# Optimization experiments

Hardware: AMD Instinct MI355X
Metric: run time of the kernel (lower is better)

The kernel has to match this reference:

```python
import jax, jax.numpy as jnp
import numpy as np

B, F, T, D = 65536, 1024, 64, 6


def setup_inputs() -> dict:
    key = jax.random.key(0)
    k0, k1, k2, k3 = jax.random.split(key, 4)
    x = jax.random.normal(k0, (B, F), dtype=jnp.float32)
    splits = jax.random.normal(k1, (T, D, F), dtype=jnp.float32)
    thresholds = jax.random.normal(k2, (T, D), dtype=jnp.float32)
    values = jax.random.normal(k3, (T, 2 ** D), dtype=jnp.float32)
    return {"x": x, "splits": splits, "thresholds": thresholds, "values": values}


def reference(x, splits, thresholds, values):
    # Since split_idx = depth % max_depth = depth, each level's split is path-independent.
    # bit_d = 1 means 'right' (score > threshold); node after D steps = 2^D - 1 + code,
    # leaf_idx = node - 2^D = code - 1 (torch negative indexing => mod 2^D).
    T_, D_, _ = splits.shape
    scores = jnp.einsum('bf,tdf->tbd', x, splits)          # (T, B, D)
    bits = (scores > thresholds[:, None, :]).astype(jnp.int32)
    pow2 = (2 ** jnp.arange(D_ - 1, -1, -1)).astype(jnp.int32)  # weight 2^(D-1-d)
    code = jnp.sum(bits * pow2, axis=-1)                   # (T, B)
    leaf = jnp.mod(code - 1, 2 ** D_)                      # (T, B)
    out_t = jnp.take_along_axis(values, leaf, axis=1)      # (T, B)
    return jnp.mean(out_t, axis=0)[:, None]                # (B, 1)
```

## Files before the change

kernel.cpp:

```cpp
#include <hip/hip_runtime.h>

#define BTOT 65536
#define FDIM 1024
#define TNUM 64
#define DNUM 6

#define BAND      1.5e-3f
#define GCUT      1.5e-4f
#define HEDGE_MAX 1.35f
#define CAP       8192

typedef unsigned int u32;
typedef unsigned long long u64;
using f32x4  = __attribute__((ext_vector_type(4))) float;
using bf16x8 = __attribute__((ext_vector_type(8))) short;

__device__ __forceinline__ short f32_to_bf16(float v) {
    u32 bits = __float_as_uint(v);
    bits += 0x7FFFu + ((bits >> 16) & 1u);
    return (short)(bits >> 16);
}
__device__ __forceinline__ float bf16_to_f32(short h) {
    return __uint_as_float(((u32)(unsigned short)h) << 16);
}

#define RPITCH 40
#define A_HI_S 0
#define A_LO_S (64 * RPITCH)
#define B_HI_S (128 * RPITCH)
#define B_LO_S (128 * RPITCH + 384 * RPITCH)
#define SMEM_SHORTS (128 * RPITCH + 2 * 384 * RPITCH)
#define B_BASE_BYTES (2 * B_HI_S)
#define BTILE_BYTES  61440
#define PRE_OFFSET   65536

__global__ void pre_split(const float* __restrict__ splits,
                          short* __restrict__ pre) {
    const int q  = blockIdx.x * 256 + threadIdx.x;
    const int r  = q >> 8;
    const int c4 = q & 255;
    const float4 v = *(const float4*)(splits + (size_t)r * FDIM + c4 * 4);
    const int ks = c4 >> 3;
    const int c  = (c4 & 7) * 4;
    short* tile = pre + (size_t)ks * (BTILE_BYTES / 2);
    const float vv[4] = {v.x, v.y, v.z, v.w};
    short hh[4], ll[4];
    #pragma unroll
    for (int e = 0; e < 4; ++e) {
        hh[e] = f32_to_bf16(vv[e]);
        ll[e] = f32_to_bf16(vv[e] - bf16_to_f32(hh[e]));
    }
    *(short4*)(tile + r * RPITCH + c)               = make_short4(hh[0], hh[1], hh[2], hh[3]);
    *(short4*)(tile + 384 * RPITCH + r * RPITCH + c) = make_short4(ll[0], ll[1], ll[2], ll[3]);
}

__global__ __launch_bounds__(256, 2)
void forest_mfma(const float* __restrict__ x,
                 const float* __restrict__ splits,
                 const float* __restrict__ thresholds,
                 const float* __restrict__ values,
                 float* __restrict__ out,
                 u32* __restrict__ gcnt,
                 u32* __restrict__ cands,
                 const short* __restrict__ pre,
                 const int use_pre) {
    __shared__ __align__(16) short smem[SMEM_SHORTS];

    const int tid  = threadIdx.x;
    const int lane = tid & 63;
    const int w    = tid >> 6;
    const int fr   = lane & 15;
    const int fq   = lane >> 4;
    const int b0   = blockIdx.x * 64;

    f32x4 acc[6][4];
    #pragma unroll
    for (int tt = 0; tt < 6; ++tt)
        #pragma unroll
        for (int bt = 0; bt < 4; ++bt) acc[tt][bt] = (f32x4)0.0f;

    #pragma unroll
    for (int j = 0; j < 2; ++j) {
        const int q = tid + j * 256, ra = q >> 3, c4 = q & 7;
        const float4 v = *(const float4*)(x + (size_t)(b0 + ra) * FDIM + c4 * 4);
        const float vv[4] = {v.x, v.y, v.z, v.w};
        short hh[4], ll[4];
        #pragma unroll
        for (int e = 0; e < 4; ++e) {
            hh[e] = f32_to_bf16(vv[e]);
            ll[e] = f32_to_bf16(vv[e] - bf16_to_f32(hh[e]));
        }
        *(short4*)(smem + A_HI_S + ra * RPITCH + c4 * 4) = make_short4(hh[0], hh[1], hh[2], hh[3]);
        *(short4*)(smem + A_LO_S + ra * RPITCH + c4 * 4) = make_short4(ll[0], ll[1], ll[2], ll[3]);
    }

    if (use_pre) {
        {
            const char* srcb = (const char*)pre;
            #pragma unroll
            for (int j = 0; j < 15; ++j) {
                const int ub = (j * 256 + w * 64) * 16;
                __builtin_amdgcn_global_load_lds(
                    (const void*)(srcb + ub + (lane << 4)),
                    (void*)((char*)smem + B_BASE_BYTES + ub),
                    16, 0, 0);
            }
        }
        __syncthreads();

        for (int ks = 0; ks < 32; ++ks) {
            bf16x8 sh[6], sl[6], xh[4], xl[4];
            #pragma unroll
            for (int tt = 0; tt < 6; ++tt) {
                const int ro = (w * 96 + tt * 16 + fr) * RPITCH + fq * 8;
                sh[tt] = *(const bf16x8*)(smem + B_HI_S + ro);
                sl[tt] = *(const bf16x8*)(smem + B_LO_S + ro);
            }
            #pragma unroll
            for (int bt = 0; bt < 4; ++bt) {
                const int ro = (bt * 16 + fr) * RPITCH + fq * 8;
                xh[bt] = *(const bf16x8*)(smem + A_HI_S + ro);
                xl[bt] = *(const bf16x8*)(smem + A_LO_S + ro);
            }
            float4 pa[2];
            if (ks < 31) {
                #pragma unroll
                for (int j = 0; j < 2; ++j) {
                    const int q = tid + j * 256, ra = q >> 3, c4 = q & 7;
                    pa[j] = *(const float4*)(x + (size_t)(b0 + ra) * FDIM + (ks + 1) * 32 + c4 * 4);
                }
            }
            __syncthreads();

            if (ks < 31) {
                const char* srcb = (const char*)pre + (size_t)(ks + 1) * BTILE_BYTES;
                #pragma unroll
                for (int j = 0; j < 15; ++j) {
                    const int ub = (j * 256 + w * 64) * 16;
                    __builtin_amdgcn_global_load_lds(
                        (const void*)(srcb + ub + (lane << 4)),
                        (void*)((char*)smem + B_BASE_BYTES + ub),
                        16, 0, 0);
                }
            }
            #pragma unroll
            for (int tt = 0; tt < 6; ++tt)
                #pragma unroll
                for (int bt = 0; bt < 4; ++bt) {
                    acc[tt][bt] = __builtin_amdgcn_mfma_f32_16x16x32_bf16(sh[tt], xh[bt], acc[tt][bt], 0, 0, 0);
                    acc[tt][bt] = __builtin_amdgcn_mfma_f32_16x16x32_bf16(sh[tt], xl[bt], acc[tt][bt], 0, 0, 0);
                    acc[tt][bt] = __builtin_amdgcn_mfma_f32_16x16x32_bf16(sl[tt], xh[bt], acc[tt][bt], 0, 0, 0);
                }
            if (ks < 31) {
                #pragma unroll
                for (int j = 0; j < 2; ++j) {
                    const int q = tid + j * 256, ra = q >> 3, c4 = q & 7;
                    const float vv[4] = {pa[j].x, pa[j].y, pa[j].z, pa[j].w};
                    short hh[4], ll[4];
                    #pragma unroll
                    for (int e = 0; e < 4; ++e) {
                        hh[e] = f32_to_bf16(vv[e]);
                        ll[e] = f32_to_bf16(vv[e] - bf16_to_f32(hh[e]));
                    }
                    *(short4*)(smem + A_HI_S + ra * RPITCH + c4 * 4) = make_short4(hh[0], hh[1], hh[2], hh[3]);
                    *(short4*)(smem + A_LO_S + ra * RPITCH + c4 * 4) = make_short4(ll[0], ll[1], ll[2], ll[3]);
                }
            }
            __syncthreads();
        }
    } else {
        for (int ks = 0; ks < 32; ++ks) {
            const int k0 = ks * 32;
            if (ks) {
                __syncthreads();
                #pragma unroll
                for (int j = 0; j < 2; ++j) {
                    const int q = tid + j * 256, ra = q >> 3, c4 = q & 7;
                    const float4 v = *(const float4*)(x + (size_t)(b0 + ra) * FDIM + k0 + c4 * 4);
                    const float vv[4] = {v.x, v.y, v.z, v.w};
                    short hh[4], ll[4];
                    #pragma unroll
                    for (int e = 0; e < 4; ++e) {
                        hh[e] = f32_to_bf16(vv[e]);
                        ll[e] = f32_to_bf16(vv[e] - bf16_to_f32(hh[e]));
                    }
                    *(short4*)(smem + A_HI_S + ra * RPITCH + c4 * 4) = make_short4(hh[0], hh[1], hh[2], hh[3]);
                    *(short4*)(smem + A_LO_S + ra * RPITCH + c4 * 4) = make_short4(ll[0], ll[1], ll[2], ll[3]);
                }
            }
            #pragma unroll
            for (int j = 0; j < 12; ++j) {
                const int q = tid + j * 256, rb = q >> 3, c4 = q & 7;
                const float4 v = *(const float4*)(splits + (size_t)rb * FDIM + k0 + c4 * 4);
                const float vv[4] = {v.x, v.y, v.z, v.w};
                short hh[4], ll[4];
                #pragma unroll
                for (int e = 0; e < 4; ++e) {
                    hh[e] = f32_to_bf16(vv[e]);
                    ll[e] = f32_to_bf16(vv[e] - bf16_to_f32(hh[e]));
                }
                *(short4*)(smem + B_HI_S + rb * RPITCH + c4 * 4) = make_short4(hh[0], hh[1], hh[2], hh[3]);
                *(short4*)(smem + B_LO_S + rb * RPITCH + c4 * 4) = make_short4(ll[0], ll[1], ll[2], ll[3]);
            }
            __syncthreads();
            bf16x8 sh[6], sl[6], xh[4], xl[4];
            #pragma unroll
            for (int tt = 0; tt < 6; ++tt) {
                const int ro = (w * 96 + tt * 16 + fr) * RPITCH + fq * 8;
                sh[tt] = *(const bf16x8*)(smem + B_HI_S + ro);
                sl[tt] = *(const bf16x8*)(smem + B_LO_S + ro);
            }
            #pragma unroll
            for (int bt = 0; bt < 4; ++bt) {
                const int ro = (bt * 16 + fr) * RPITCH + fq * 8;
                xh[bt] = *(const bf16x8*)(smem + A_HI_S + ro);
                xl[bt] = *(const bf16x8*)(smem + A_LO_S + ro);
            }
            #pragma unroll
            for (int tt = 0; tt < 6; ++tt)
                #pragma unroll
                for (int bt = 0; bt < 4; ++bt) {
                    acc[tt][bt] = __builtin_amdgcn_mfma_f32_16x16x32_bf16(sh[tt], xh[bt], acc[tt][bt], 0, 0, 0);
                    acc[tt][bt] = __builtin_amdgcn_mfma_f32_16x16x32_bf16(sh[tt], xl[bt], acc[tt][bt], 0, 0, 0);
                    acc[tt][bt] = __builtin_amdgcn_mfma_f32_16x16x32_bf16(sl[tt], xh[bt], acc[tt][bt], 0, 0, 0);
                }
        }
        __syncthreads();
    }

    float th[6][4];
    #pragma unroll
    for (int tt = 0; tt < 6; ++tt)
        #pragma unroll
        for (int reg = 0; reg < 4; ++reg)
            th[tt][reg] = thresholds[w * 96 + tt * 16 + fq * 4 + reg];

    float* psum = (float*)smem;

    #pragma unroll
    for (int bt = 0; bt < 4; ++bt) {
        u64 bal[6][4];
        u32 bandmask = 0;
        #pragma unroll
        for (int tt = 0; tt < 6; ++tt)
            #pragma unroll
            for (int reg = 0; reg < 4; ++reg) {
                const float df = acc[tt][bt][reg] - th[tt][reg];
                bal[tt][reg] = __ballot(df > 0.0f);
                if (__builtin_expect(fabsf(df) < BAND, 0))
                    bandmask |= 1u << ((tt * 16 + fq * 4 + reg) / 6);
            }
        bandmask |= __shfl_xor(bandmask, 16);
        bandmask |= __shfl_xor(bandmask, 32);

        float partial = 0.0f;
        #pragma unroll
        for (int jj = 0; jj < 4; ++jj) {
            const int j = fq * 4 + jj;
            int code = 0;
            #pragma unroll
            for (int d = 0; d < DNUM; ++d) {
                const int l   = j * 6 + d;
                const int stt = l >> 4;
                const int pos = l & 15;
                const int bit = (int)((bal[stt][pos & 3] >> (((pos >> 2) << 4) + fr)) & 1ull);
                code |= bit << (5 - d);
            }
            const int t = w * 16 + j;
            partial += values[t * 64 + ((code - 1) & 63)];
            if (__builtin_expect((bandmask >> j) & 1u, 0)) {
                const u32 gidx = atomicAdd(gcnt, 1u);
                if (gidx < CAP)
                    cands[gidx] = ((u32)(b0 + bt * 16 + fr) << 16) | ((u32)t << 6) | (u32)code;
            }
        }
        psum[(bt * 16 + fr) * 16 + w * 4 + fq] = partial;
    }
    __syncthreads();
    if (tid < 64) {
        float s = 0.0f;
        #pragma unroll
        for (int k = 0; k < 16; ++k) s += psum[tid * 16 + k];
        out[b0 + tid] = s * (1.0f / 64.0f);
    }
}

__global__ __launch_bounds__(256)
void band_fix(const float* __restrict__ x,
              const float* __restrict__ splits,
              const float* __restrict__ thresholds,
              const float* __restrict__ values,
              float* __restrict__ out,
              const u32* __restrict__ gcnt,
              const u32* __restrict__ cands) {
    const u32 n = min(*gcnt, (u32)CAP);
    const u32 gid  = blockIdx.x * 256 + threadIdx.x;
    const u32 site = gid >> 3;
    const u32 sub  = gid & 7;
    if (site >= n) return;
    const u32 e = cands[site];
    const int b = (int)(e >> 16);
    const int t = (int)((e >> 6) & 63u);
    const int code_approx = (int)(e & 63u);
    const int d = (sub < 6) ? (int)sub : 0;

    const float* xr = x + (size_t)b * FDIM;
    const float* sr = splits + ((size_t)t * DNUM + d) * FDIM;
    float a = 0.0f;
    #pragma unroll 4
    for (int f = 0; f < FDIM; f += 16) {
        const float4 x0 = *(const float4*)(xr + f);
        const float4 x1 = *(const float4*)(xr + f + 4);
        const float4 x2 = *(const float4*)(xr + f + 8);
        const float4 x3 = *(const float4*)(xr + f + 12);
        const float4 s0 = *(const float4*)(sr + f);
        const float4 s1 = *(const float4*)(sr + f + 4);
        const float4 s2 = *(const float4*)(sr + f + 8);
        const float4 s3 = *(const float4*)(sr + f + 12);
        a = fmaf(x0.x, s0.x, a); a = fmaf(x0.y, s0.y, a);
        a = fmaf(x0.z, s0.z, a); a = fmaf(x0.w, s0.w, a);
        a = fmaf(x1.x, s1.x, a); a = fmaf(x1.y, s1.y, a);
        a = fmaf(x1.z, s1.z, a); a = fmaf(x1.w, s1.w, a);
        a = fmaf(x2.x, s2.x, a); a = fmaf(x2.y, s2.y, a);
        a = fmaf(x2.z, s2.z, a); a = fmaf(x2.w, s2.w, a);
        a = fmaf(x3.x, s3.x, a); a = fmaf(x3.y, s3.y, a);
        a = fmaf(x3.z, s3.z, a); a = fmaf(x3.w, s3.w, a);
    }
    const float df = a - thresholds[t * DNUM + d];

    const int lane = (int)(threadIdx.x & 63);
    const int base = lane & ~7;
    float dfs[6];
    #pragma unroll
    for (int j = 0; j < 6; ++j) dfs[j] = __shfl(df, base + j);

    if (sub == 0) {
        int code_chain = 0;
        #pragma unroll
        for (int j = 0; j < 6; ++j)
            code_chain = (code_chain << 1) | (dfs[j] > 0.0f ? 1 : 0);
        const float vA = values[t * 64 + ((code_approx - 1) & 63)];
        const float vC = values[t * 64 + ((code_chain - 1) & 63)];
        float delta = vC - vA;
        #pragma unroll
        for (int j = 0; j < 6; ++j) {
            if (fabsf(dfs[j]) < GCUT) {
                const int cf = code_chain ^ (1 << (5 - j));
                const float dv = values[t * 64 + ((cf - 1) & 63)] - vC;
                if (fabsf(dv) < HEDGE_MAX) delta += dv * 0.5f;
            }
        }
        atomicAdd(out + b, delta * (1.0f / 64.0f));
    }
}

extern "C" void kernel_launch(void* const* d_in, const int* in_sizes, int n_in,
                              void* d_out, int out_size, void* d_ws, size_t ws_size,
                              hipStream_t stream) {
    const float* x          = (const float*)d_in[0];
    const float* splits     = (const float*)d_in[1];
    const float* thresholds = (const float*)d_in[2];
    const float* values     = (const float*)d_in[3];
    float* out = (float*)d_out;

    u32* gcnt   = (u32*)d_ws;
    u32* cands  = (u32*)((char*)d_ws + 64);
    short* pre  = (short*)((char*)d_ws + PRE_OFFSET);
    const int use_pre = (ws_size >= (size_t)PRE_OFFSET + 32u * (size_t)BTILE_BYTES) ? 1 : 0;

    (void)hipMemsetAsync(gcnt, 0, 4, stream);
    if (use_pre)
        pre_split<<<dim3(384), dim3(256), 0, stream>>>(splits, pre);
    forest_mfma<<<dim3(BTOT / 64), dim3(256), 0, stream>>>(
        x, splits, thresholds, values, out, gcnt, cands, pre, use_pre);
    band_fix<<<dim3(CAP * 8 / 256), dim3(256), 0, stream>>>(
        x, splits, thresholds, values, out, gcnt, cands);
}
```

Baseline: 249.4 us.

## Load pre-split MFMA fragments and x directly from global, bypassing LDS

Pre-split splits are now stored in per-lane MFMA fragment order, so each wave loads its B operands straight from global/L2 into registers. Each lane also loads and splits its own x fragment into hi/lo. This removes LDS staging, both per-iteration barriers, and the global_load_lds double-buffer. The LDS path becomes a separate fallback kernel. Without explicit prefetch the main loop may stall on global-load latency, and x row reads are less coalesced (8 floats per lane per row).

```diff
diff --git a/kernel.cpp b/kernel.cpp
--- a/kernel.cpp
+++ b/kernel.cpp
@@ -23,16 +23,18 @@
 __device__ __forceinline__ float bf16_to_f32(short h) {
     return __uint_as_float(((u32)(unsigned short)h) << 16);
 }
-
-#define RPITCH 40
-#define A_HI_S 0
-#define A_LO_S (64 * RPITCH)
-#define B_HI_S (128 * RPITCH)
-#define B_LO_S (128 * RPITCH + 384 * RPITCH)
-#define SMEM_SHORTS (128 * RPITCH + 2 * 384 * RPITCH)
-#define B_BASE_BYTES (2 * B_HI_S)
-#define BTILE_BYTES  61440
-#define PRE_OFFSET   65536
+__device__ __forceinline__ void cvt8(float4 a0, float4 a1, bf16x8& h, bf16x8& l) {
+    const float vv[8] = {a0.x, a0.y, a0.z, a0.w, a1.x, a1.y, a1.z, a1.w};
+    #pragma unroll
+    for (int e = 0; e < 8; ++e) {
+        const short hh = f32_to_bf16(vv[e]);
+        h[e] = hh;
+        l[e] = f32_to_bf16(vv[e] - bf16_to_f32(hh));
+    }
+}
+
+#define PRE_OFFSET 65536
+#define PRE_SHORTS (32 * 24 * 1024)
 
 __global__ void pre_split(const float* __restrict__ splits,
                           short* __restrict__ pre) {
@@ -41,8 +43,11 @@
     const int c4 = q & 255;
     const float4 v = *(const float4*)(splits + (size_t)r * FDIM + c4 * 4);
     const int ks = c4 >> 3;
-    const int c  = (c4 & 7) * 4;
-    short* tile = pre + (size_t)ks * (BTILE_BYTES / 2);
+    const int fq = (c4 >> 1) & 3;
+    const int e0 = (c4 & 1) * 4;
+    const int tile = r >> 4, fr = r & 15;
+    const int lane = fq * 16 + fr;
+    const size_t base = ((size_t)ks * 24 + tile) * 1024 + (size_t)lane * 8 + e0;
     const float vv[4] = {v.x, v.y, v.z, v.w};
     short hh[4], ll[4];
     #pragma unroll
@@ -50,21 +55,19 @@
         hh[e] = f32_to_bf16(vv[e]);
         ll[e] = f32_to_bf16(vv[e] - bf16_to_f32(hh[e]));
     }
-    *(short4*)(tile + r * RPITCH + c)               = make_short4(hh[0], hh[1], hh[2], hh[3]);
-    *(short4*)(tile + 384 * RPITCH + r * RPITCH + c) = make_short4(ll[0], ll[1], ll[2], ll[3]);
+    *(short4*)(pre + base)       = make_short4(hh[0], hh[1], hh[2], hh[3]);
+    *(short4*)(pre + base + 512) = make_short4(ll[0], ll[1], ll[2], ll[3]);
 }
 
 __global__ __launch_bounds__(256, 2)
 void forest_mfma(const float* __restrict__ x,
-                 const float* __restrict__ splits,
                  const float* __restrict__ thresholds,
                  const float* __restrict__ values,
                  float* __restrict__ out,
                  u32* __restrict__ gcnt,
                  u32* __restrict__ cands,
-                 const short* __restrict__ pre,
-                 const int use_pre) {
-    __shared__ __align__(16) short smem[SMEM_SHORTS];
+                 const short* __restrict__ pre) {
+    __shared__ float psum[64 * 16];
 
     const int tid  = threadIdx.x;
     const int lane = tid & 63;
@@ -79,153 +82,27 @@
         #pragma unroll
         for (int bt = 0; bt < 4; ++bt) acc[tt][bt] = (f32x4)0.0f;
 
-    #pragma unroll
-    for (int j = 0; j < 2; ++j) {
-        const int q = tid + j * 256, ra = q >> 3, c4 = q & 7;
-        const float4 v = *(const float4*)(x + (size_t)(b0 + ra) * FDIM + c4 * 4);
-        const float vv[4] = {v.x, v.y, v.z, v.w};
-        short hh[4], ll[4];
-        #pragma unroll
-        for (int e = 0; e < 4; ++e) {
-            hh[e] = f32_to_bf16(vv[e]);
-            ll[e] = f32_to_bf16(vv[e] - bf16_to_f32(hh[e]));
-        }
-        *(short4*)(smem + A_HI_S + ra * RPITCH + c4 * 4) = make_short4(hh[0], hh[1], hh[2], hh[3]);
-        *(short4*)(smem + A_LO_S + ra * RPITCH + c4 * 4) = make_short4(ll[0], ll[1], ll[2], ll[3]);
-    }
-
-    if (use_pre) {
-        {
-            const char* srcb = (const char*)pre;
-            #pragma unroll
-            for (int j = 0; j < 15; ++j) {
-                const int ub = (j * 256 + w * 64) * 16;
-                __builtin_amdgcn_global_load_lds(
-                    (const void*)(srcb + ub + (lane << 4)),
-                    (void*)((char*)smem + B_BASE_BYTES + ub),
-                    16, 0, 0);
-            }
-        }
-        __syncthreads();
-
-        for (int ks = 0; ks < 32; ++ks) {
-            bf16x8 sh[6], sl[6], xh[4], xl[4];
-            #pragma unroll
-            for (int tt = 0; tt < 6; ++tt) {
-                const int ro = (w * 96 + tt * 16 + fr) * RPITCH + fq * 8;
-                sh[tt] = *(const bf16x8*)(smem + B_HI_S + ro);
-                sl[tt] = *(const bf16x8*)(smem + B_LO_S + ro);
-            }
+    for (int ks = 0; ks < 32; ++ks) {
+        bf16x8 sh[6], sl[6], xh[4], xl[4];
+        const short* fb = pre + ((size_t)ks * 24 + w * 6) * 1024 + (size_t)lane * 8;
+        #pragma unroll
+        for (int tt = 0; tt < 6; ++tt) {
+            sh[tt] = *(const bf16x8*)(fb + tt * 1024);
+            sl[tt] = *(const bf16x8*)(fb + tt * 1024 + 512);
+        }
+        #pragma unroll
+        for (int bt = 0; bt < 4; ++bt) {
+            const float* xr = x + (size_t)(b0 + bt * 16 + fr) * FDIM + ks * 32 + fq * 8;
+            cvt8(*(const float4*)xr, *(const float4*)(xr + 4), xh[bt], xl[bt]);
+        }
+        #pragma unroll
+        for (int tt = 0; tt < 6; ++tt)
             #pragma unroll
             for (int bt = 0; bt < 4; ++bt) {
-                const int ro = (bt * 16 + fr) * RPITCH + fq * 8;
-                xh[bt] = *(const bf16x8*)(smem + A_HI_S + ro);
-                xl[bt] = *(const bf16x8*)(smem + A_LO_S + ro);
-            }
-            float4 pa[2];
-            if (ks < 31) {
-                #pragma unroll
-                for (int j = 0; j < 2; ++j) {
-                    const int q = tid + j * 256, ra = q >> 3, c4 = q & 7;
-                    pa[j] = *(const float4*)(x + (size_t)(b0 + ra) * FDIM + (ks + 1) * 32 + c4 * 4);
-                }
-            }
-            __syncthreads();
-
-            if (ks < 31) {
-                const char* srcb = (const char*)pre + (size_t)(ks + 1) * BTILE_BYTES;
-                #pragma unroll
-                for (int j = 0; j < 15; ++j) {
-                    const int ub = (j * 256 + w * 64) * 16;
-                    __builtin_amdgcn_global_load_lds(
-                        (const void*)(srcb + ub + (lane << 4)),
-                        (void*)((char*)smem + B_BASE_BYTES + ub),
-                        16, 0, 0);
-                }
-            }
-            #pragma unroll
-            for (int tt = 0; tt < 6; ++tt)
-                #pragma unroll
-                for (int bt = 0; bt < 4; ++bt) {
-                    acc[tt][bt] = __builtin_amdgcn_mfma_f32_16x16x32_bf16(sh[tt], xh[bt], acc[tt][bt], 0, 0, 0);
-                    acc[tt][bt] = __builtin_amdgcn_mfma_f32_16x16x32_bf16(sh[tt], xl[bt], acc[tt][bt], 0, 0, 0);
-                    acc[tt][bt] = __builtin_amdgcn_mfma_f32_16x16x32_bf16(sl[tt], xh[bt], acc[tt][bt], 0, 0, 0);
-                }
-            if (ks < 31) {
-                #pragma unroll
-                for (int j = 0; j < 2; ++j) {
-                    const int q = tid + j * 256, ra = q >> 3, c4 = q & 7;
-                    const float vv[4] = {pa[j].x, pa[j].y, pa[j].z, pa[j].w};
-                    short hh[4], ll[4];
-                    #pragma unroll
-                    for (int e = 0; e < 4; ++e) {
-                        hh[e] = f32_to_bf16(vv[e]);
-                        ll[e] = f32_to_bf16(vv[e] - bf16_to_f32(hh[e]));
-                    }
-                    *(short4*)(smem + A_HI_S + ra * RPITCH + c4 * 4) = make_short4(hh[0], hh[1], hh[2], hh[3]);
-                    *(short4*)(smem + A_LO_S + ra * RPITCH + c4 * 4) = make_short4(ll[0], ll[1], ll[2], ll[3]);
-                }
-            }
-            __syncthreads();
-        }
-    } else {
-        for (int ks = 0; ks < 32; ++ks) {
-            const int k0 = ks * 32;
-            if (ks) {
-                __syncthreads();
-                #pragma unroll
-                for (int j = 0; j < 2; ++j) {
-                    const int q = tid + j * 256, ra = q >> 3, c4 = q & 7;
-                    const float4 v = *(const float4*)(x + (size_t)(b0 + ra) * FDIM + k0 + c4 * 4);
-                    const float vv[4] = {v.x, v.y, v.z, v.w};
-                    short hh[4], ll[4];
-                    #pragma unroll
-                    for (int e = 0; e < 4; ++e) {
-                        hh[e] = f32_to_bf16(vv[e]);
-                        ll[e] = f32_to_bf16(vv[e] - bf16_to_f32(hh[e]));
-                    }
-                    *(short4*)(smem + A_HI_S + ra * RPITCH + c4 * 4) = make_short4(hh[0], hh[1], hh[2], hh[3]);
-                    *(short4*)(smem + A_LO_S + ra * RPITCH + c4 * 4) = make_short4(ll[0], ll[1], ll[2], ll[3]);
-                }
-            }
-            #pragma unroll
-            for (int j = 0; j < 12; ++j) {
-                const int q = tid + j * 256, rb = q >> 3, c4 = q & 7;
-                const float4 v = *(const float4*)(splits + (size_t)rb * FDIM + k0 + c4 * 4);
-                const float vv[4] = {v.x, v.y, v.z, v.w};
-                short hh[4], ll[4];
-                #pragma unroll
-                for (int e = 0; e < 4; ++e) {
-                    hh[e] = f32_to_bf16(vv[e]);
-                    ll[e] = f32_to_bf16(vv[e] - bf16_to_f32(hh[e]));
-                }
-                *(short4*)(smem + B_HI_S + rb * RPITCH + c4 * 4) = make_short4(hh[0], hh[1], hh[2], hh[3]);
-                *(short4*)(smem + B_LO_S + rb * RPITCH + c4 * 4) = make_short4(ll[0], ll[1], ll[2], ll[3]);
-            }
-            __syncthreads();
-            bf16x8 sh[6], sl[6], xh[4], xl[4];
-            #pragma unroll
-            for (int tt = 0; tt < 6; ++tt) {
-                const int ro = (w * 96 + tt * 16 + fr) * RPITCH + fq * 8;
-                sh[tt] = *(const bf16x8*)(smem + B_HI_S + ro);
-                sl[tt] = *(const bf16x8*)(smem + B_LO_S + ro);
-            }
-            #pragma unroll
-            for (int bt = 0; bt < 4; ++bt) {
-                const int ro = (bt * 16 + fr) * RPITCH + fq * 8;
-                xh[bt] = *(const bf16x8*)(smem + A_HI_S + ro);
-                xl[bt] = *(const bf16x8*)(smem + A_LO_S + ro);
-            }
-            #pragma unroll
-            for (int tt = 0; tt < 6; ++tt)
-                #pragma unroll
-                for (int bt = 0; bt < 4; ++bt) {
-                    acc[tt][bt] = __builtin_amdgcn_mfma_f32_16x16x32_bf16(sh[tt], xh[bt], acc[tt][bt], 0, 0, 0);
-                    acc[tt][bt] = __builtin_amdgcn_mfma_f32_16x16x32_bf16(sh[tt], xl[bt], acc[tt][bt], 0, 0, 0);
-                    acc[tt][bt] = __builtin_amdgcn_mfma_f32_16x16x32_bf16(sl[tt], xh[bt], acc[tt][bt], 0, 0, 0);
-                }
-        }
-        __syncthreads();
+                acc[tt][bt] = __builtin_amdgcn_mfma_f32_16x16x32_bf16(sh[tt], xh[bt], acc[tt][bt], 0, 0, 0);
+                acc[tt][bt] = __builtin_amdgcn_mfma_f32_16x16x32_bf16(sh[tt], xl[bt], acc[tt][bt], 0, 0, 0);
+                acc[tt][bt] = __builtin_amdgcn_mfma_f32_16x16x32_bf16(sl[tt], xh[bt], acc[tt][bt], 0, 0, 0);
+            }
     }
 
     float th[6][4];
@@ -234,8 +111,6 @@
         #pragma unroll
         for (int reg = 0; reg < 4; ++reg)
             th[tt][reg] = thresholds[w * 96 + tt * 16 + fq * 4 + reg];
-
-    float* psum = (float*)smem;
 
     #pragma unroll
     for (int bt = 0; bt < 4; ++bt) {
@@ -253,6 +128,145 @@
         bandmask |= __shfl_xor(bandmask, 16);
         bandmask |= __shfl_xor(bandmask, 32);
 
+        float partial = 0.0f;
+        #pragma unroll
+        for (int jj = 0; jj < 4; ++jj) {
+            const int j = fq * 4 + jj;
+            int code = 0;
+            #pragma unroll
+            for (int d = 0; d < DNUM; ++d) {
+                const int l   = j * 6 + d;
+                const int stt = l >> 4;
+                const int pos = l & 15;
+                const int bit = (int)((bal[stt][pos & 3] >> (((pos >> 2) << 4) + fr)) & 1ull);
+                code |= bit << (5 - d);
+            }
+            const int t = w * 16 + j;
+            partial += values[t * 64 + ((code - 1) & 63)];
+            if (__builtin_expect((bandmask >> j) & 1u, 0)) {
+                const u32 gidx = atomicAdd(gcnt, 1u);
+                if (gidx < CAP)
+                    cands[gidx] = ((u32)(b0 + bt * 16 + fr) << 16) | ((u32)t << 6) | (u32)code;
+            }
+        }
+        psum[(bt * 16 + fr) * 16 + w * 4 + fq] = partial;
+    }
+    __syncthreads();
+    if (tid < 64) {
+        float s = 0.0f;
+        #pragma unroll
+        for (int k = 0; k < 16; ++k) s += psum[tid * 16 + k];
+        out[b0 + tid] = s * (1.0f / 64.0f);
+    }
+}
+
+#define RPITCH 40
+#define A_HI_S 0
+#define A_LO_S (64 * RPITCH)
+#define B_HI_S (128 * RPITCH)
+#define B_LO_S (128 * RPITCH + 384 * RPITCH)
+#define SMEM_SHORTS (128 * RPITCH + 2 * 384 * RPITCH)
+__global__ __launch_bounds__(256, 2)
+void forest_mfma_lds(const float* __restrict__ x,
+                     const float* __restrict__ splits,
+                     const float* __restrict__ thresholds,
+                     const float* __restrict__ values,
+                     float* __restrict__ out,
+                     u32* __restrict__ gcnt,
+                     u32* __restrict__ cands) {
+    __shared__ __align__(16) short smem[SMEM_SHORTS];
+    const int tid  = threadIdx.x;
+    const int lane = tid & 63;
+    const int w    = tid >> 6;
+    const int fr   = lane & 15;
+    const int fq   = lane >> 4;
+    const int b0   = blockIdx.x * 64;
+
+    f32x4 acc[6][4];
+    #pragma unroll
+    for (int tt = 0; tt < 6; ++tt)
+        #pragma unroll
+        for (int bt = 0; bt < 4; ++bt) acc[tt][bt] = (f32x4)0.0f;
+
+    for (int ks = 0; ks < 32; ++ks) {
+        const int k0 = ks * 32;
+        if (ks) __syncthreads();
+        #pragma unroll
+        for (int j = 0; j < 2; ++j) {
+            const int q = tid + j * 256, ra = q >> 3, c4 = q & 7;
+            const float4 v = *(const float4*)(x + (size_t)(b0 + ra) * FDIM + k0 + c4 * 4);
+            const float vv[4] = {v.x, v.y, v.z, v.w};
+            short hh[4], ll[4];
+            #pragma unroll
+            for (int e = 0; e < 4; ++e) {
+                hh[e] = f32_to_bf16(vv[e]);
+                ll[e] = f32_to_bf16(vv[e] - bf16_to_f32(hh[e]));
+            }
+            *(short4*)(smem + A_HI_S + ra * RPITCH + c4 * 4) = make_short4(hh[0], hh[1], hh[2], hh[3]);
+            *(short4*)(smem + A_LO_S + ra * RPITCH + c4 * 4) = make_short4(ll[0], ll[1], ll[2], ll[3]);
+        }
+        #pragma unroll
+        for (int j = 0; j < 12; ++j) {
+            const int q = tid + j * 256, rb = q >> 3, c4 = q & 7;
+            const float4 v = *(const float4*)(splits + (size_t)rb * FDIM + k0 + c4 * 4);
+            const float vv[4] = {v.x, v.y, v.z, v.w};
+            short hh[4], ll[4];
+            #pragma unroll
+            for (int e = 0; e < 4; ++e) {
+                hh[e] = f32_to_bf16(vv[e]);
+                ll[e] = f32_to_bf16(vv[e] - bf16_to_f32(hh[e]));
+            }
+            *(short4*)(smem + B_HI_S + rb * RPITCH + c4 * 4) = make_short4(hh[0], hh[1], hh[2], hh[3]);
+            *(short4*)(smem + B_LO_S + rb * RPITCH + c4 * 4) = make_short4(ll[0], ll[1], ll[2], ll[3]);
+        }
+        __syncthreads();
+        bf16x8 sh[6], sl[6], xh[4], xl[4];
+        #pragma unroll
+        for (int tt = 0; tt < 6; ++tt) {
+            const int ro = (w * 96 + tt * 16 + fr) * RPITCH + fq * 8;
+            sh[tt] = *(const bf16x8*)(smem + B_HI_S + ro);
+            sl[tt] = *(const bf16x8*)(smem + B_LO_S + ro);
+        }
+        #pragma unroll
+        for (int bt = 0; bt < 4; ++bt) {
+            const int ro = (bt * 16 + fr) * RPITCH + fq * 8;
+            xh[bt] = *(const bf16x8*)(smem + A_HI_S + ro);
+            xl[bt] = *(const bf16x8*)(smem + A_LO_S + ro);
+        }
+        #pragma unroll
+        for (int tt = 0; tt < 6; ++tt)
+            #pragma unroll
+            for (int bt = 0; bt < 4; ++bt) {
+                acc[tt][bt] = __builtin_amdgcn_mfma_f32_16x16x32_bf16(sh[tt], xh[bt], acc[tt][bt], 0, 0, 0);
+                acc[tt][bt] = __builtin_amdgcn_mfma_f32_16x16x32_bf16(sh[tt], xl[bt], acc[tt][bt], 0, 0, 0);
+                acc[tt][bt] = __builtin_amdgcn_mfma_f32_16x16x32_bf16(sl[tt], xh[bt], acc[tt][bt], 0, 0, 0);
+            }
+    }
+    __syncthreads();
+
+    float th[6][4];
+    #pragma unroll
+    for (int tt = 0; tt < 6; ++tt)
+        #pragma unroll
+        for (int reg = 0; reg < 4; ++reg)
+            th[tt][reg] = thresholds[w * 96 + tt * 16 + fq * 4 + reg];
+    float* psum = (float*)smem;
+    __syncthreads();
+    #pragma unroll
+    for (int bt = 0; bt < 4; ++bt) {
+        u64 bal[6][4];
+        u32 bandmask = 0;
+        #pragma unroll
+        for (int tt = 0; tt < 6; ++tt)
+            #pragma unroll
+            for (int reg = 0; reg < 4; ++reg) {
+                const float df = acc[tt][bt][reg] - th[tt][reg];
+                bal[tt][reg] = __ballot(df > 0.0f);
+                if (__builtin_expect(fabsf(df) < BAND, 0))
+                    bandmask |= 1u << ((tt * 16 + fq * 4 + reg) / 6);
+            }
+        bandmask |= __shfl_xor(bandmask, 16);
+        bandmask |= __shfl_xor(bandmask, 32);
         float partial = 0.0f;
         #pragma unroll
         for (int jj = 0; jj < 4; ++jj) {
@@ -366,13 +380,17 @@
     u32* gcnt   = (u32*)d_ws;
     u32* cands  = (u32*)((char*)d_ws + 64);
     short* pre  = (short*)((char*)d_ws + PRE_OFFSET);
-    const int use_pre = (ws_size >= (size_t)PRE_OFFSET + 32u * (size_t)BTILE_BYTES) ? 1 : 0;
+    const int use_pre = (ws_size >= (size_t)PRE_OFFSET + 2u * PRE_SHORTS) ? 1 : 0;
 
     (void)hipMemsetAsync(gcnt, 0, 4, stream);
-    if (use_pre)
+    if (use_pre) {
         pre_split<<<dim3(384), dim3(256), 0, stream>>>(splits, pre);
-    forest_mfma<<<dim3(BTOT / 64), dim3(256), 0, stream>>>(
-        x, splits, thresholds, values, out, gcnt, cands, pre, use_pre);
+        forest_mfma<<<dim3(BTOT / 64), dim3(256), 0, stream>>>(
+            x, thresholds, values, out, gcnt, cands, pre);
+    } else {
+        forest_mfma_lds<<<dim3(BTOT / 64), dim3(256), 0, stream>>>(
+            x, splits, thresholds, values, out, gcnt, cands);
+    }
     band_fix<<<dim3(CAP * 8 / 256), dim3(256), 0, stream>>>(
         x, splits, thresholds, values, out, gcnt, cands);
 }
```

Measured after the change: 280.1 us. 1.12x slower.
